# Kernel tuning notes

Hardware: AMD Instinct MI355X
Metric: run time of the kernel (lower is better)

Reference implementation:

```python
import jax, jax.numpy as jnp
import numpy as np

# Static module configuration (from init_kwargs / input_specs)
N, S, D, d, B = 256, 2, 64, 2, 64
NOUT = int(np.ceil((N - 1) / S) + 1)  # 129
NIN = N - NOUT                         # 127
EPS = 1e-60
STDDEV = 0.5


def setup_inputs() -> dict:
    key = jax.random.key(0)
    k1, k2, k3 = jax.random.split(key, 3)
    return {
        "inp": jax.random.normal(k1, (N, B, d), jnp.float32),
        "mps_input": jax.random.normal(k2, (NIN, D, D, d), jnp.float32) * STDDEV,
        "mps_output": jax.random.normal(k3, (NOUT, D, D, d, d), jnp.float32) * STDDEV,
        "training": 0,
    }


def _divide_no_nan(x, y):
    y_safe = jnp.where(y == 0, jnp.ones_like(y), y)
    return jnp.where(y == 0, jnp.zeros_like(x), x / y_safe)


def _log_norm(mps_input, mps_output):
    # Sequential transfer-matrix scan over all N sites (no samples fixed).
    Al = jnp.zeros((D, D), jnp.float32).at[0, 0].set(1.0)
    scals = []
    i_in = 0
    for i in range(N):
        amax = jnp.max(jnp.abs(Al))
        Al = Al / amax
        scals.append(amax)
        if i % S == 0 or i == N - 1:
            M = mps_output[NOUT - 1] if i == N - 1 else mps_output[i // S]  # [D,D,d,d]
            T = jnp.einsum('du,dkij->kuij', Al, M)
            Al = jnp.einsum('kuij,ulij->kl', T, M)
        else:
            M = mps_input[i_in]  # [D,D,d]
            T = jnp.einsum('du,dki->kui', Al, M)
            Al = jnp.einsum('kui,uli->kl', T, M)
            i_in += 1
    scals.append(Al[0, 0])
    return jnp.sum(jnp.log(jnp.stack(scals)))


def _forward(inp, mps_input, mps_output):
    # --- build batched site MPS (inference path: training=False, no dropout) ---
    A = jnp.einsum('bi,lrij->blrj', inp[0], mps_output[0, :1])  # [B,1,D,d]
    mps = [A]
    i_in = 0
    Al = None
    out_S = []
    for i in range(1, N - 1):
        if i % S == 0:
            x = jnp.einsum('bi,lrij->blrj', inp[i], mps_output[i // S])  # [B,D,D,d]
            A = jnp.einsum('blr,brdi->bldi', Al, x)
            Al = None
            mps.append(A)
        else:
            A = jnp.einsum('bi,lri->blr', inp[i], mps_input[i_in])  # [B,D,D]
            Al = A if Al is None else jnp.einsum('blr,brd->bld', Al, A)
            amax = jnp.max(jnp.abs(Al), axis=(1, 2), keepdims=True)
            Al = _divide_no_nan(Al, amax)
            out_S.append(amax.reshape(-1))
            i_in += 1
    x = jnp.einsum('bi,lrij->blrj', inp[N - 1], mps_output[-1][:, :1])  # [B,D,1,d]
    A = jnp.einsum('blr,brdi->bldi', Al, x) if Al is not None else x
    mps.append(A)
    out_S = 2.0 * jnp.sum(jnp.log(jnp.stack(out_S, axis=-1) + EPS), axis=1)  # [B]

    # --- contract <psi|psi> chain with per-step rescaling ---
    scals = []
    A0 = mps[0][:, 0]  # [B,D,d]
    Al = jnp.einsum('bui,bdi->bud', A0, A0)
    amax = jnp.max(jnp.abs(Al), axis=(1, 2), keepdims=True)
    Al = _divide_no_nan(Al, amax)
    scals.append(amax.reshape(-1))
    for A in mps[1:]:
        T = jnp.einsum('bdu,bdli->blui', Al, A)
        Al = jnp.einsum('blui,buri->blr', T, A)
        amax = jnp.max(jnp.abs(Al), axis=(1, 2), keepdims=True)
        Al = _divide_no_nan(Al, amax)
        scals.append(amax.reshape(-1))
    log_contr = jnp.sum(jnp.log(jnp.stack(scals, axis=-1) + EPS), axis=1)  # [B]
    logp = log_contr + jnp.log(jnp.abs(Al[:, 0, 0]) + EPS) + out_S
    return logp - _log_norm(mps_input, mps_output)


def reference(inp, mps_input, mps_output, training):
    # training==0 -> dropout disabled (faithful to call(..., training=False))
    return _forward(inp, mps_input, mps_output)
```

## Files before the change

kernel.cpp:

```cpp
#include <hip/hip_runtime.h>
#include <math.h>


typedef __attribute__((ext_vector_type(8))) short short8;
typedef __attribute__((ext_vector_type(4))) float f32x4;

#define MFMA16(a, b, c) __builtin_amdgcn_mfma_f32_16x16x32_bf16(a, b, c, 0, 0, 0)

#define ST 72
#define PL 4608
#define BS 72
#define L_AL(q) ((q) * PL)
#define L_MF(p) (2 * PL + (p) * 18432)
#define L_T     (2 * PL + 2 * 18432)
#define SU_U16  65024
#define BPL(i) ((i) * PL)

#define MINB 0ull
#define MOTB 1040384ull
#define MFIB 3153920ull
#define MFOB 4194304ull
#define WS_U16_TOT 6307840ull
#define EXPFW WS_U16_TOT
#define EXPBW (WS_U16_TOT + 4096ull)
#define EXPAF (WS_U16_TOT + 8192ull)
#define EXPW  (EXPAF + 262144ull)
#define WS_U16_ALL (EXPW + 262144ull)

#define BARRIER() do { asm volatile("s_waitcnt lgkmcnt(0)" ::: "memory"); \
                       __builtin_amdgcn_s_barrier(); } while (0)

__device__ __forceinline__ unsigned pk2(float lo, float hi) {
    unsigned r;
    asm("v_cvt_pk_bf16_f32 %0, %1, %2" : "=v"(r) : "v"(lo), "v"(hi));
    return r;
}
__device__ __forceinline__ ushort f2b(float f) {
    union { float f; unsigned u; } x; x.f = f;
    return (ushort)((x.u + 0x7FFFu + ((x.u >> 16) & 1u)) >> 16);
}
__device__ __forceinline__ float b2f(ushort h) {
    union { unsigned u; float f; } x; x.u = ((unsigned)h) << 16; return x.f;
}
__device__ __forceinline__ short8 ldfrag(const ushort* p) {
    return *reinterpret_cast<const short8*>(p);
}
__device__ __forceinline__ void st64(ushort* p, unsigned lo, unsigned hi) {
    unsigned long long v = ((unsigned long long)hi << 32) | (unsigned long long)lo;
    *reinterpret_cast<unsigned long long*>(p) = v;
}
__device__ __forceinline__ float wave_max(float v) {
#pragma unroll
    for (int off = 32; off > 0; off >>= 1) v = fmaxf(v, __shfl_xor(v, off, 64));
    return v;
}
__device__ __forceinline__ float blk_max(float v, float* scr, int tid) {
    v = wave_max(v);
    BARRIER();
    if ((tid & 63) == 0) scr[tid >> 6] = v;
    BARRIER();
    return fmaxf(fmaxf(scr[0], scr[1]), fmaxf(scr[2], scr[3]));
}
__device__ __forceinline__ short8 pk8(const float* v) {
    union { short8 s; unsigned u[4]; } r;
    r.u[0] = pk2(v[0], v[1]); r.u[1] = pk2(v[2], v[3]);
    r.u[2] = pk2(v[4], v[5]); r.u[3] = pk2(v[6], v[7]);
    return r.s;
}

__global__ __launch_bounds__(256) void preconv(const float* __restrict__ mi,
                                               const float* __restrict__ mo,
                                               ushort* __restrict__ wsb) {
    __shared__ float lf[16384];
    const int tid = threadIdx.x, blk = blockIdx.x;
    if (blk < 127) {
        const float* src = mi + (size_t)blk * 8192;
#pragma unroll
        for (int n = 0; n < 8; n++)
            *reinterpret_cast<f32x4*>(lf + 4 * (tid + 256 * n)) =
                *reinterpret_cast<const f32x4*>(src + 4 * (tid + 256 * n));
        __syncthreads();
        ushort* d1 = wsb + MINB + (size_t)blk * 8192;
        ushort* d2 = wsb + MFIB + (size_t)blk * 8192;
        const bool adj = (blk >= 64);
#pragma unroll
        for (int n = 0; n < 4; n++) {
            int c = tid + 256 * n;
            float va[8], vb[8];
            int rp = c >> 3, d0 = (c & 7) * 8;
#pragma unroll
            for (int r = 0; r < 8; r++) {
                va[r] = lf[8 * c + r];
                if (!adj) {
                    int msrc = (rp & 63) * 2 + (rp >> 6);
                    vb[r] = lf[(d0 + r) * 128 + msrc];
                } else {
                    vb[r] = lf[(rp & 63) * 128 + (d0 + r) * 2 + (rp >> 6)];
                }
            }
            *reinterpret_cast<short8*>(d1 + 8 * c) = pk8(va);
            *reinterpret_cast<short8*>(d2 + 8 * c) = pk8(vb);
        }
    } else {
        int s = blk - 127;
        const float* src = mo + (size_t)s * 16384;
#pragma unroll
        for (int n = 0; n < 16; n++)
            *reinterpret_cast<f32x4*>(lf + 4 * (tid + 256 * n)) =
                *reinterpret_cast<const f32x4*>(src + 4 * (tid + 256 * n));
        __syncthreads();
        ushort* d1 = wsb + MOTB + (size_t)s * 16384;
        ushort* d2 = wsb + MFOB + (size_t)s * 16384;
        const bool adj = (s >= 64);
#pragma unroll
        for (int n = 0; n < 8; n++) {
            int c = tid + 256 * n;
            float va[8], vb[8];
            int j = c >> 10, r = (c >> 4) & 63, dg = c & 15;
            int rp = c >> 3, d0 = (c & 7) * 8;
#pragma unroll
            for (int q = 0; q < 4; q++)
#pragma unroll
                for (int i = 0; i < 2; i++)
                    va[q * 2 + i] = lf[(dg * 4 + q) * 256 + r * 4 + i * 2 + j];
#pragma unroll
            for (int rr = 0; rr < 8; rr++) {
                if (!adj) {
                    int msrc = (rp & 63) * 4 + (rp >> 6);
                    vb[rr] = lf[(d0 + rr) * 256 + msrc];
                } else {
                    vb[rr] = lf[(rp & 63) * 256 + (d0 + rr) * 4 + (rp >> 6)];
                }
            }
            *reinterpret_cast<short8*>(d1 + 8 * c) = pk8(va);
            *reinterpret_cast<short8*>(d2 + 8 * c) = pk8(vb);
        }
    }
}

__device__ __forceinline__ void ldbf1(short8 (&bf1)[2][4], const ushort* __restrict__ mfg,
                                      int nq, int tid) {
    const int w = tid >> 6, g = (tid >> 4) & 3, l15 = tid & 15;
#pragma unroll
    for (int ks = 0; ks < 2; ks++)
#pragma unroll
        for (int tc = 0; tc < 4; tc++)
            if (tc < nq)
                bf1[ks][tc] = ldfrag(mfg + (size_t)(64 * tc + 16 * w + l15) * 64 + 32 * ks + 8 * g);
}
template <int QW, bool BFS>
__device__ __forceinline__ void ln_mm1(ushort* su, const short8 (&bf1)[2][4],
                                       int q, int p, float sc, int tid) {
    constexpr int TSx = QW * BS + 8;
    const int w = tid >> 6, g = (tid >> 4) & 3, l15 = tid & 15;
    const f32x4 fz = {0.f, 0.f, 0.f, 0.f};
    f32x4 acc[4][QW];
#pragma unroll
    for (int tr = 0; tr < 4; tr++)
#pragma unroll
        for (int tc = 0; tc < QW; tc++) acc[tr][tc] = fz;
#pragma unroll
    for (int ks = 0; ks < 2; ks++) {
        short8 bf[QW];
#pragma unroll
        for (int tc = 0; tc < QW; tc++) {
            if constexpr (BFS) bf[tc] = bf1[ks][tc];
            else bf[tc] = ldfrag(su + L_MF(p) + (64 * tc + 16 * w + l15) * ST + 32 * ks + 8 * g);
        }
#pragma unroll
        for (int tr = 0; tr < 4; tr++) {
            short8 af = ldfrag(su + L_AL(q) + (16 * tr + l15) * ST + 32 * ks + 8 * g);
#pragma unroll
            for (int tc = 0; tc < QW; tc++) acc[tr][tc] = MFMA16(af, bf[tc], acc[tr][tc]);
        }
    }
#pragma unroll
    for (int tr = 0; tr < 4; tr++)
#pragma unroll
        for (int tc = 0; tc < QW; tc++)
            st64(&su[L_T + (16 * w + l15) * TSx + tc * BS + 16 * tr + 4 * g],
                 pk2(acc[tr][tc][0] * sc, acc[tr][tc][1] * sc),
                 pk2(acc[tr][tc][2] * sc, acc[tr][tc][3] * sc));
}
template <int QW>
__device__ __forceinline__ void ln_mm2_reg(ushort* su, const short8 (&bf1)[2][4],
                                           int p, int tid, float* redw) {
    constexpr int TSx = QW * BS + 8;
    const int w = tid >> 6, g = (tid >> 4) & 3, l15 = tid & 15;
    const f32x4 fz = {0.f, 0.f, 0.f, 0.f};
    f32x4 acc[4];
#pragma unroll
    for (int tr = 0; tr < 4; tr++) acc[tr] = fz;
#pragma unroll
    for (int ks2 = 0; ks2 < 2 * QW; ks2++) {
        const short8 bf = bf1[ks2 & 1][ks2 >> 1];
#pragma unroll
        for (int tr = 0; tr < 4; tr++) {
            short8 af = ldfrag(su + L_T + (16 * tr + l15) * TSx + (ks2 >> 1) * BS +
                               (ks2 & 1) * 32 + 8 * g);
            acc[tr] = MFMA16(af, bf, acc[tr]);
        }
    }
    float lm = 0.f;
#pragma unroll
    for (int tr = 0; tr < 4; tr++)
#pragma unroll
        for (int r2 = 0; r2 < 4; r2++) lm = fmaxf(lm, fabsf(acc[tr][r2]));
    lm = wave_max(lm);
    if ((tid & 63) == 0) redw[w] = lm;
#pragma unroll
    for (int tr = 0; tr < 4; tr++)
        st64(&su[L_AL(p ^ 1) + (16 * w + l15) * ST + 16 * tr + 4 * g],
             pk2(acc[tr][0], acc[tr][1]), pk2(acc[tr][2], acc[tr][3]));
}
template <int QW>
__device__ __forceinline__ void ln_mm2_lds(ushort* su, int q, int p, int tid, float* red) {
    constexpr int TSx = QW * BS + 8;
    const int w = tid >> 6, g = (tid >> 4) & 3, l15 = tid & 15;
    const f32x4 fz = {0.f, 0.f, 0.f, 0.f};
    f32x4 acc[4];
#pragma unroll
    for (int tc = 0; tc < 4; tc++) acc[tc] = fz;
#pragma unroll
    for (int ks2 = 0; ks2 < 2 * QW; ks2++) {
        short8 af = ldfrag(su + L_T + (16 * w + l15) * TSx + (ks2 >> 1) * BS + (ks2 & 1) * 32 + 8 * g);
#pragma unroll
        for (int tc = 0; tc < 4; tc++) {
            short8 bf = ldfrag(su + L_MF(p) + (((ks2 >> 1) << 6) + 16 * tc + l15) * ST +
                               (ks2 & 1) * 32 + 8 * g);
            acc[tc] = MFMA16(af, bf, acc[tc]);
        }
    }
    float lm = 0.f;
#pragma unroll
    for (int tc = 0; tc < 4; tc++)
#pragma unroll
        for (int r2 = 0; r2 < 4; r2++) lm = fmaxf(lm, fabsf(acc[tc][r2]));
    lm = wave_max(lm);
    if ((tid & 63) == 0) red[w] = lm;
#pragma unroll
    for (int tc = 0; tc < 4; tc++)
        st64(&su[L_AL(q ^ 1) + (16 * tc + l15) * ST + 16 * w + 4 * g],
             pk2(acc[tc][0], acc[tc][1]), pk2(acc[tc][2], acc[tc][3]));
}
template <int QWN>
__device__ __forceinline__ void ln_stage_raw(ushort* su, int pn, const float* __restrict__ Mg, int tid) {
    const int a63 = tid & 63, hi = tid >> 6;
#pragma unroll
    for (int n = 0; n < 4 * QWN; n++) {
        int mb = hi + 4 * n;
        f32x4 v = *reinterpret_cast<const f32x4*>(Mg + 4 * ((size_t)a63 * (16 * QWN) + mb));
#pragma unroll
        for (int c = 0; c < 4; c++) {
            int m = 4 * mb + c;
            int rp = (m & (QWN - 1)) * 64 + (m / QWN);
            su[L_MF(pn) + rp * ST + a63] = f2b(v[c]);
        }
    }
}

__device__ __forceinline__ void bt_mm1(ushort* su, int tid) {
    const int w = tid >> 6, g = (tid >> 4) & 3, l15 = tid & 15;
    const f32x4 fz = {0.f, 0.f, 0.f, 0.f};
    f32x4 acc[2][4];
#pragma unroll
    for (int j = 0; j < 2; j++)
#pragma unroll
        for (int tr = 0; tr < 4; tr++) acc[j][tr] = fz;
#pragma unroll
    for (int ks = 0; ks < 2; ks++) {
        short8 q0 = ldfrag(su + BPL(1) + (16 * w + l15) * ST + 32 * ks + 8 * g);
        short8 q1 = ldfrag(su + BPL(2) + (16 * w + l15) * ST + 32 * ks + 8 * g);
#pragma unroll
        for (int tr = 0; tr < 4; tr++) {
            short8 pA = ldfrag(su + BPL(0) + (16 * tr + l15) * ST + 32 * ks + 8 * g);
            acc[0][tr] = MFMA16(pA, q0, acc[0][tr]);
            acc[1][tr] = MFMA16(pA, q1, acc[1][tr]);
        }
    }
#pragma unroll
    for (int j = 0; j < 2; j++)
#pragma unroll
        for (int tr = 0; tr < 4; tr++)
            st64(&su[BPL(3 + j) + (16 * w + l15) * ST + 16 * tr + 4 * g],
                 pk2(acc[j][tr][0], acc[j][tr][1]), pk2(acc[j][tr][2], acc[j][tr][3]));
}
__device__ __forceinline__ void bw_mm1(ushort* su, int tid) {
    const int w = tid >> 6, g = (tid >> 4) & 3, l15 = tid & 15;
    const f32x4 fz = {0.f, 0.f, 0.f, 0.f};
    f32x4 acc[2][4];
#pragma unroll
    for (int j = 0; j < 2; j++)
#pragma unroll
        for (int tr = 0; tr < 4; tr++) acc[j][tr] = fz;
#pragma unroll
    for (int ks = 0; ks < 2; ks++) {
        short8 bAin = ldfrag(su + BPL(0) + (16 * w + l15) * ST + 32 * ks + 8 * g);
#pragma unroll
        for (int tr = 0; tr < 4; tr++) {
            short8 x0 = ldfrag(su + BPL(1) + (16 * tr + l15) * ST + 32 * ks + 8 * g);
            short8 x1 = ldfrag(su + BPL(2) + (16 * tr + l15) * ST + 32 * ks + 8 * g);
            acc[0][tr] = MFMA16(x0, bAin, acc[0][tr]);
            acc[1][tr] = MFMA16(x1, bAin, acc[1][tr]);
        }
    }
#pragma unroll
    for (int j = 0; j < 2; j++)
#pragma unroll
        for (int tr = 0; tr < 4; tr++)
            st64(&su[BPL(3 + j) + (16 * w + l15) * ST + 16 * tr + 4 * g],
                 pk2(acc[j][tr][0], acc[j][tr][1]), pk2(acc[j][tr][2], acc[j][tr][3]));
}
__device__ __forceinline__ void bt_mm2(ushort* su, float sc, int tid) {
    const int w = tid >> 6, g = (tid >> 4) & 3, l15 = tid & 15;
    const f32x4 fz = {0.f, 0.f, 0.f, 0.f};
    f32x4 acc[2][4];
#pragma unroll
    for (int j = 0; j < 2; j++)
#pragma unroll
        for (int tr = 0; tr < 4; tr++) acc[j][tr] = fz;
#pragma unroll
    for (int ks = 0; ks < 2; ks++) {
        short8 q0 = ldfrag(su + BPL(3) + (16 * w + l15) * ST + 32 * ks + 8 * g);
        short8 q1 = ldfrag(su + BPL(4) + (16 * w + l15) * ST + 32 * ks + 8 * g);
#pragma unroll
        for (int tr = 0; tr < 4; tr++) {
            short8 pA = ldfrag(su + BPL(7) + (16 * tr + l15) * ST + 32 * ks + 8 * g);
            acc[0][tr] = MFMA16(pA, q0, acc[0][tr]);
            acc[1][tr] = MFMA16(pA, q1, acc[1][tr]);
        }
    }
#pragma unroll
    for (int j = 0; j < 2; j++)
#pragma unroll
        for (int tr = 0; tr < 4; tr++)
            st64(&su[BPL(5 + j) + (16 * w + l15) * ST + 16 * tr + 4 * g],
                 pk2(acc[j][tr][0] * sc, acc[j][tr][1] * sc),
                 pk2(acc[j][tr][2] * sc, acc[j][tr][3] * sc));
}
__device__ __forceinline__ void bt_mm3(ushort* su, int tid, float* redw) {
    const int w = tid >> 6, g = (tid >> 4) & 3, l15 = tid & 15;
    const f32x4 fz = {0.f, 0.f, 0.f, 0.f};
    f32x4 acc[4];
#pragma unroll
    for (int tc = 0; tc < 4; tc++) acc[tc] = fz;
#pragma unroll
    for (int j = 0; j < 2; j++)
#pragma unroll
        for (int ks = 0; ks < 2; ks++) {
            short8 pT = ldfrag(su + BPL(5 + j) + (16 * w + l15) * ST + 32 * ks + 8 * g);
#pragma unroll
            for (int tc = 0; tc < 4; tc++) {
                short8 qf = ldfrag(su + BPL(3 + j) + (16 * tc + l15) * ST + 32 * ks + 8 * g);
                acc[tc] = MFMA16(pT, qf, acc[tc]);
            }
        }
    float lm = 0.f;
#pragma unroll
    for (int tc = 0; tc < 4; tc++)
#pragma unroll
        for (int r2 = 0; r2 < 4; r2++) lm = fmaxf(lm, fabsf(acc[tc][r2]));
    lm = wave_max(lm);
    if ((tid & 63) == 0) redw[w] = lm;
#pragma unroll
    for (int tc = 0; tc < 4; tc++)
        st64(&su[BPL(7) + (16 * tc + l15) * ST + 16 * w + 4 * g],
             pk2(acc[tc][0], acc[tc][1]), pk2(acc[tc][2], acc[tc][3]));
}

template <bool BFS>
__global__ __launch_bounds__(256, 1) void proj_chain(
    const float* __restrict__ inp, const float* __restrict__ mps_in,
    const float* __restrict__ mps_out, float* __restrict__ wsf,
    ushort* __restrict__ wsb) {
    __shared__ __align__(16) ushort su[SU_U16];
    __shared__ float fsc[176];
    float* red = fsc;
    float* bms = fsc + 16;
    float* A0s = fsc + 32;
    const int tid = threadIdx.x;

    if (blockIdx.x >= 128) {
        if constexpr (BFS) {
            const bool fw = (blockIdx.x == 128);
#pragma unroll
            for (int n = 0; n < 9; n++)
                reinterpret_cast<unsigned*>(su)[tid + 256 * n] = 0u;
            if (tid == 0) su[0] = (ushort)0x3F80;
            auto wq = [&](int s) -> int {
                if (fw) return (s & 1) ? 2 : 4;
                int site = 255 - s;
                return (((site & 1) == 0) || site == 255) ? 4 : 2;
            };
            auto wp = [&](int s) -> const ushort* {
                if (fw) return (s & 1) ? wsb + MFIB + (size_t)(s >> 1) * 8192
                                       : wsb + MFOB + (size_t)(s >> 1) * 16384;
                int site = 255 - s;
                if (site == 255) return wsb + MFOB + 128ull * 16384;
                if ((site & 1) == 0) return wsb + MFOB + (size_t)(site >> 1) * 16384;
                return wsb + MFIB + (size_t)(site >> 1) * 8192;
            };
            short8 bfA[2][4], bfB[2][4];
            ldbf1(bfA, wp(0), wq(0), tid);
            BARRIER();
            float accl = 0.f;
            auto lnstep = [&](int s_, short8 (&CUR)[2][4], short8 (&NXT)[2][4]) {
                int p_ = s_ & 1;
                float sc_ = 1.f;
                if (s_ > 0) {
                    float* rb_ = red + p_ * 8;
                    float m4_ = fmaxf(fmaxf(rb_[0], rb_[1]), fmaxf(rb_[2], rb_[3]));
                    sc_ = 1.f / m4_;
                    if (tid == 0) accl += logf(m4_);
                }
                int q_ = wq(s_);
                if (q_ == 4) ln_mm1<4, true>(su, CUR, p_, p_, sc_, tid);
                else         ln_mm1<2, true>(su, CUR, p_, p_, sc_, tid);
                if (s_ + 1 < 128) ldbf1(NXT, wp(s_ + 1), wq(s_ + 1), tid);
                BARRIER();
                if (q_ == 4) ln_mm2_reg<4>(su, CUR, p_, tid, red + ((s_ + 1) & 1) * 8);
                else         ln_mm2_reg<2>(su, CUR, p_, tid, red + ((s_ + 1) & 1) * 8);
                BARRIER();
            };
            for (int t = 0; t < 64; ++t) {
                lnstep(2 * t, bfA, bfB);
                lnstep(2 * t + 1, bfB, bfA);
            }
            size_t base = fw ? EXPFW : EXPBW;
            int row = tid >> 2, c0 = (tid & 3) * 16;
            *reinterpret_cast<short8*>(wsb + base + row * 64 + c0) =
                ldfrag(su + (size_t)row * ST + c0);
            *reinterpret_cast<short8*>(wsb + base + row * 64 + c0 + 8) =
                ldfrag(su + (size_t)row * ST + c0 + 8);
            if (tid == 0) wsf[fw ? 128 : 129] = accl;
            return;
        } else {
            if (blockIdx.x == 129) return;
#pragma unroll
            for (int n = 0; n < 9; n++)
                reinterpret_cast<unsigned*>(su)[tid + 256 * n] = 0u;
            if (tid == 0) su[0] = (ushort)0x3F80;
            short8 bfd[2][4];
            ln_stage_raw<4>(su, 0, mps_out, tid);
            BARRIER();
            float accl = 0.f;
            for (int i = 0; i < 256; i++) {
                int p = i & 1;
                int qw = (((i & 1) == 0) || i == 255) ? 4 : 2;
                float sc = 1.f;
                if (i > 0) {
                    float* rb = red + (i & 1) * 8;
                    float m4 = fmaxf(fmaxf(rb[0], rb[1]), fmaxf(rb[2], rb[3]));
                    sc = 1.f / m4;
                    if (tid == 0) accl += logf(m4);
                }
                if (qw == 4) ln_mm1<4, false>(su, bfd, p, p, sc, tid);
                else         ln_mm1<2, false>(su, bfd, p, p, sc, tid);
                int j = i + 1;
                if (j < 256) {
                    int qn = (((j & 1) == 0) || j == 255) ? 4 : 2;
                    if (qn == 4)
                        ln_stage_raw<4>(su, p ^ 1,
                                        mps_out + (size_t)16384 * ((j == 255) ? 128 : (j >> 1)), tid);
                    else
                        ln_stage_raw<2>(su, p ^ 1, mps_in + (size_t)8192 * (j >> 1), tid);
                }
                if (qw == 4) ln_mm2_lds<4>(su, p, p, tid, red + ((i + 1) & 1) * 8);
                else         ln_mm2_lds<2>(su, p, p, tid, red + ((i + 1) & 1) * 8);
                BARRIER();
            }
            if (tid == 0) { accl += logf(b2f(su[L_AL(0)])); wsf[128] = accl; }
            return;
        }
    }

    if (!BFS && blockIdx.x >= 64) return;
    const bool FWD = (blockIdx.x < 64);
    const int b = blockIdx.x & 63;
    float accl = 0.f;
    short8 pfA[4], pfX[8];

    auto loadpf = [&](int k2) {
        const ushort* mb = wsb + MINB + (size_t)(k2 - 1) * 8192;
        const ushort* xb = wsb + MOTB + (size_t)k2 * 16384;
#pragma unroll
        for (int n = 0; n < 4; n++)
            pfA[n] = *reinterpret_cast<const short8*>(mb + (size_t)(tid + 256 * n) * 8);
#pragma unroll
        for (int n = 0; n < 8; n++)
            pfX[n] = *reinterpret_cast<const short8*>(xb + (size_t)((n >> 2) * 1024 + tid + 256 * (n & 3)) * 8);
    };
    auto stage_bf = [&](int k2) {
        float jv0 = inp[((2 * k2 - 1) * 64 + b) * 2], jv1 = inp[((2 * k2 - 1) * 64 + b) * 2 + 1];
        float ov0 = inp[((2 * k2) * 64 + b) * 2],     ov1 = inp[((2 * k2) * 64 + b) * 2 + 1];
#pragma unroll
        for (int n = 0; n < 4; n++) {
            int c = tid + 256 * n, l = c >> 4, dd0 = (c & 15) * 4;
            short8 r8 = pfA[n];
            float v0 = jv0 * b2f((ushort)r8[0]) + jv1 * b2f((ushort)r8[1]);
            float v1 = jv0 * b2f((ushort)r8[2]) + jv1 * b2f((ushort)r8[3]);
            float v2 = jv0 * b2f((ushort)r8[4]) + jv1 * b2f((ushort)r8[5]);
            float v3 = jv0 * b2f((ushort)r8[6]) + jv1 * b2f((ushort)r8[7]);
            st64(&su[BPL(0) + l * ST + dd0], pk2(v0, v1), pk2(v2, v3));
        }
#pragma unroll
        for (int n = 0; n < 8; n++) {
            int j = n >> 2, c = tid + 256 * (n & 3), r = c >> 4, dd0 = (c & 15) * 4;
            short8 r8 = pfX[n];
            float v0 = ov0 * b2f((ushort)r8[0]) + ov1 * b2f((ushort)r8[1]);
            float v1 = ov0 * b2f((ushort)r8[2]) + ov1 * b2f((ushort)r8[3]);
            float v2 = ov0 * b2f((ushort)r8[4]) + ov1 * b2f((ushort)r8[5]);
            float v3 = ov0 * b2f((ushort)r8[6]) + ov1 * b2f((ushort)r8[7]);
            st64(&su[BPL(1 + j) + r * ST + dd0], pk2(v0, v1), pk2(v2, v3));
        }
    };
    auto stage_f32 = [&](int k2) {
        const int a63 = tid & 63, hi2 = tid >> 6;
        const float* Min = mps_in + (size_t)(k2 - 1) * 8192;
        const float* Mo  = mps_out + (size_t)k2 * 16384;
        float jv0 = inp[((2 * k2 - 1) * 64 + b) * 2], jv1 = inp[((2 * k2 - 1) * 64 + b) * 2 + 1];
        float ov0 = inp[((2 * k2) * 64 + b) * 2],     ov1 = inp[((2 * k2) * 64 + b) * 2 + 1];
#pragma unroll
        for (int n = 0; n < 8; n++) {
            int f = tid + 256 * n, l = f >> 5, dd = (2 * f) & 63;
            f32x4 v = *reinterpret_cast<const f32x4*>(Min + 4 * f);
            *reinterpret_cast<unsigned*>(&su[BPL(0) + l * ST + dd]) =
                pk2(jv0 * v[0] + jv1 * v[1], jv0 * v[2] + jv1 * v[3]);
        }
#pragma unroll
        for (int n = 0; n < 16; n++) {
            int r = hi2 + 4 * n;
            f32x4 v = *reinterpret_cast<const f32x4*>(Mo + 4 * ((size_t)a63 * 64 + r));
            su[BPL(1) + r * ST + a63] = f2b(ov0 * v[0] + ov1 * v[2]);
            su[BPL(2) + r * ST + a63] = f2b(ov0 * v[1] + ov1 * v[3]);
        }
    };
    auto init_state = [&](const float* Msrc, float v0, float v1) {
        if (tid < 128) {
            int r = tid >> 1, jj = tid & 1;
            A0s[tid] = v0 * Msrc[r * 256 * 0 + r * 0 + 0] ;
        }
    };

    const int nt = FWD ? 64 : 63;
    auto sidx = [&](int t) { return FWD ? (1 + t) : (127 - t); };

    if constexpr (BFS) loadpf(sidx(0));
    {
        const float* Ms;
        float v0, v1;
        int rstride;
        if (FWD) { Ms = mps_out; v0 = inp[b * 2]; v1 = inp[b * 2 + 1]; rstride = 4; }
        else { Ms = mps_out + (size_t)128 * 16384; v0 = inp[(255 * 64 + b) * 2];
               v1 = inp[(255 * 64 + b) * 2 + 1]; rstride = 256; }
        if (tid < 128) {
            int r = tid >> 1, jj = tid & 1;
            A0s[tid] = v0 * Ms[r * rstride + jj] + v1 * Ms[r * rstride + 2 + jj];
        }
        BARRIER();
        float vals[16];
        float lm = 0.f;
#pragma unroll
        for (int n = 0; n < 16; n++) {
            int e = tid + 256 * n;
            int u = e >> 6, d2 = e & 63;
            float v = A0s[2 * u] * A0s[2 * d2] + A0s[2 * u + 1] * A0s[2 * d2 + 1];
            vals[n] = v;
            lm = fmaxf(lm, fabsf(v));
        }
        float amax = blk_max(lm, bms, tid);
        if (tid == 0) accl += logf(amax);
        float sc0 = (amax > 0.f) ? 1.f / amax : 0.f;
#pragma unroll
        for (int n = 0; n < 16; n++) {
            int e = tid + 256 * n;
            su[BPL(7) + (e >> 6) * ST + (e & 63)] = f2b(vals[n] * sc0);
        }
    }
    if (tid < 4) red[tid] = 1.0f;
    const int kmax = FWD ? (BFS ? 64 : 127) : 0;
    const int NT = BFS ? nt : 127;
    if constexpr (BFS) {
        stage_bf(sidx(0));
        if (NT > 1) loadpf(sidx(1));
    } else {
        stage_f32(1);
    }
    BARRIER();

    for (int t = 0; t < NT; t++) {
        int rb = t & 1;
        if (FWD) bt_mm1(su, tid);
        else     bw_mm1(su, tid);
        {
            float* r4 = red + rb * 4;
            float m4 = fmaxf(fmaxf(r4[0], r4[1]), fmaxf(r4[2], r4[3]));
            float sc = 1.f / m4;
            if (tid == 0) accl += logf(m4);
            bt_mm2(su, sc, tid);
        }
        BARRIER();
        if (t + 1 < NT) {
            if constexpr (BFS) stage_bf(sidx(t + 1));
            else               stage_f32(t + 2);
        }
        bt_mm3(su, tid, red + (rb ^ 1) * 4);
        if constexpr (BFS) { if (t + 2 < NT) loadpf(sidx(t + 2)); }
        BARRIER();
    }

    if constexpr (BFS) {
        size_t base = (FWD ? EXPAF : EXPW) + (size_t)b * 4096;
        int row = tid >> 2, c0 = (tid & 3) * 16;
        *reinterpret_cast<short8*>(wsb + base + row * 64 + c0) =
            ldfrag(su + BPL(7) + (size_t)row * ST + c0);
        *reinterpret_cast<short8*>(wsb + base + row * 64 + c0 + 8) =
            ldfrag(su + BPL(7) + (size_t)row * ST + c0 + 8);
        if (tid == 0) wsf[FWD ? b : 64 + b] = accl;
    } else {
        const float* Mo128 = mps_out + (size_t)128 * 16384;
        float fv0 = inp[(255 * 64 + b) * 2], fv1 = inp[(255 * 64 + b) * 2 + 1];
        if (tid < 128) {
            int d2 = tid >> 1, jj = tid & 1;
            A0s[tid] = fv0 * Mo128[d2 * 256 + jj] + fv1 * Mo128[d2 * 256 + 2 + jj];
        }
        BARRIER();
        float part = 0.f;
#pragma unroll
        for (int n = 0; n < 16; n++) {
            int e = tid + 256 * n;
            int d2 = e >> 6, u = e & 63;
            part += b2f(su[BPL(7) + d2 * ST + u]) *
                    (A0s[2 * d2] * A0s[2 * u] + A0s[2 * d2 + 1] * A0s[2 * u + 1]);
        }
#pragma unroll
        for (int off = 32; off > 0; off >>= 1)
            part += __shfl_xor(part, off, 64);
        BARRIER();
        if ((tid & 63) == 0) bms[tid >> 6] = part;
        BARRIER();
        if (tid == 0) {
            float v = bms[0] + bms[1] + bms[2] + bms[3];
            wsf[b] = accl + logf(fabsf(v));
        }
    }
}

__global__ void proj_combine(const float* __restrict__ wsf, const ushort* __restrict__ wsb,
                             float* __restrict__ out, int n, int mode) {
    __shared__ float sred[8];
    const int b = blockIdx.x, tid = threadIdx.x;
    if (b >= n) return;
    if (!mode) {
        if (tid == 0) out[b] = wsf[b] - wsf[128];
        return;
    }
    float d1 = 0.f, d2 = 0.f;
#pragma unroll
    for (int q = 0; q < 16; q++) {
        int e = tid + 256 * q;
        d1 += b2f(wsb[EXPAF + (size_t)b * 4096 + e]) * b2f(wsb[EXPW + (size_t)b * 4096 + e]);
        d2 += b2f(wsb[EXPFW + e]) * b2f(wsb[EXPBW + e]);
    }
#pragma unroll
    for (int off = 32; off > 0; off >>= 1) {
        d1 += __shfl_xor(d1, off, 64);
        d2 += __shfl_xor(d2, off, 64);
    }
    if ((tid & 63) == 0) { sred[tid >> 6] = d1; sred[4 + (tid >> 6)] = d2; }
    __syncthreads();
    if (tid == 0) {
        float D1 = sred[0] + sred[1] + sred[2] + sred[3];
        float D2 = sred[4] + sred[5] + sred[6] + sred[7];
        out[b] = wsf[b] + wsf[64 + b] + logf(fabsf(D1)) -
                 (wsf[128] + wsf[129] + logf(fabsf(D2)));
    }
}

extern "C" void kernel_launch(void* const* d_in, const int* in_sizes, int n_in,
                              void* d_out, int out_size, void* d_ws, size_t ws_size,
                              hipStream_t stream) {
    const float* inp = (const float*)d_in[0];
    const float* mi  = (const float*)d_in[1];
    const float* mo  = (const float*)d_in[2];
    float* wsf = (float*)d_ws;
    ushort* wsb = (ushort*)((char*)d_ws + 1024);
    size_t need = 1024 + WS_U16_ALL * 2;
    int mode = (ws_size >= need) ? 1 : 0;
    if (mode) {
        preconv<<<dim3(256), dim3(256), 0, stream>>>(mi, mo, wsb);
        proj_chain<true><<<dim3(130), dim3(256), 0, stream>>>(inp, mi, mo, wsf, wsb);
    } else {
        proj_chain<false><<<dim3(130), dim3(256), 0, stream>>>(inp, mi, mo, wsf, wsb);
    }
    proj_combine<<<dim3(64), dim3(256), 0, stream>>>(wsf, wsb, (float*)d_out, out_size, mode);
}
```

Before: 316.1 us.

## Stage log-norm weights through LDS with register prefetch, split MFMA accumulators

The log-norm scan blocks stop holding the site weights as per-wave register fragments loaded straight from global memory. They now stage each site's weights into a double-buffered LDS slot, prefetching the site two steps ahead into registers. The second matmul reads weights from LDS, which leaves one barrier per step instead of two. The mm2 and bt_mm3 kernels also split their MFMA accumulation into two independent chains to shorten dependency stalls, at the cost of extra registers and an add. Unused helper code is removed.

```diff
diff --git a/kernel.cpp b/kernel.cpp
--- a/kernel.cpp
+++ b/kernel.cpp
@@ -138,17 +138,7 @@
     }
 }
 
-__device__ __forceinline__ void ldbf1(short8 (&bf1)[2][4], const ushort* __restrict__ mfg,
-                                      int nq, int tid) {
-    const int w = tid >> 6, g = (tid >> 4) & 3, l15 = tid & 15;
-#pragma unroll
-    for (int ks = 0; ks < 2; ks++)
-#pragma unroll
-        for (int tc = 0; tc < 4; tc++)
-            if (tc < nq)
-                bf1[ks][tc] = ldfrag(mfg + (size_t)(64 * tc + 16 * w + l15) * 64 + 32 * ks + 8 * g);
-}
-template <int QW, bool BFS>
+template <int QW, bool REGW>
 __device__ __forceinline__ void ln_mm1(ushort* su, const short8 (&bf1)[2][4],
                                        int q, int p, float sc, int tid) {
     constexpr int TSx = QW * BS + 8;
@@ -164,7 +154,7 @@
         short8 bf[QW];
 #pragma unroll
         for (int tc = 0; tc < QW; tc++) {
-            if constexpr (BFS) bf[tc] = bf1[ks][tc];
+            if constexpr (REGW) bf[tc] = bf1[ks][tc];
             else bf[tc] = ldfrag(su + L_MF(p) + (64 * tc + 16 * w + l15) * ST + 32 * ks + 8 * g);
         }
 #pragma unroll
@@ -181,46 +171,15 @@
             st64(&su[L_T + (16 * w + l15) * TSx + tc * BS + 16 * tr + 4 * g],
                  pk2(acc[tr][tc][0] * sc, acc[tr][tc][1] * sc),
                  pk2(acc[tr][tc][2] * sc, acc[tr][tc][3] * sc));
-}
-template <int QW>
-__device__ __forceinline__ void ln_mm2_reg(ushort* su, const short8 (&bf1)[2][4],
-                                           int p, int tid, float* redw) {
-    constexpr int TSx = QW * BS + 8;
-    const int w = tid >> 6, g = (tid >> 4) & 3, l15 = tid & 15;
-    const f32x4 fz = {0.f, 0.f, 0.f, 0.f};
-    f32x4 acc[4];
-#pragma unroll
-    for (int tr = 0; tr < 4; tr++) acc[tr] = fz;
-#pragma unroll
-    for (int ks2 = 0; ks2 < 2 * QW; ks2++) {
-        const short8 bf = bf1[ks2 & 1][ks2 >> 1];
-#pragma unroll
-        for (int tr = 0; tr < 4; tr++) {
-            short8 af = ldfrag(su + L_T + (16 * tr + l15) * TSx + (ks2 >> 1) * BS +
-                               (ks2 & 1) * 32 + 8 * g);
-            acc[tr] = MFMA16(af, bf, acc[tr]);
-        }
-    }
-    float lm = 0.f;
-#pragma unroll
-    for (int tr = 0; tr < 4; tr++)
-#pragma unroll
-        for (int r2 = 0; r2 < 4; r2++) lm = fmaxf(lm, fabsf(acc[tr][r2]));
-    lm = wave_max(lm);
-    if ((tid & 63) == 0) redw[w] = lm;
-#pragma unroll
-    for (int tr = 0; tr < 4; tr++)
-        st64(&su[L_AL(p ^ 1) + (16 * w + l15) * ST + 16 * tr + 4 * g],
-             pk2(acc[tr][0], acc[tr][1]), pk2(acc[tr][2], acc[tr][3]));
 }
 template <int QW>
 __device__ __forceinline__ void ln_mm2_lds(ushort* su, int q, int p, int tid, float* red) {
     constexpr int TSx = QW * BS + 8;
     const int w = tid >> 6, g = (tid >> 4) & 3, l15 = tid & 15;
     const f32x4 fz = {0.f, 0.f, 0.f, 0.f};
-    f32x4 acc[4];
-#pragma unroll
-    for (int tc = 0; tc < 4; tc++) acc[tc] = fz;
+    f32x4 accA[4], accB[4];
+#pragma unroll
+    for (int tc = 0; tc < 4; tc++) { accA[tc] = fz; accB[tc] = fz; }
 #pragma unroll
     for (int ks2 = 0; ks2 < 2 * QW; ks2++) {
         short8 af = ldfrag(su + L_T + (16 * w + l15) * TSx + (ks2 >> 1) * BS + (ks2 & 1) * 32 + 8 * g);
@@ -228,9 +187,13 @@
         for (int tc = 0; tc < 4; tc++) {
             short8 bf = ldfrag(su + L_MF(p) + (((ks2 >> 1) << 6) + 16 * tc + l15) * ST +
                                (ks2 & 1) * 32 + 8 * g);
-            acc[tc] = MFMA16(af, bf, acc[tc]);
-        }
-    }
+            if (ks2 & 1) accB[tc] = MFMA16(af, bf, accB[tc]);
+            else         accA[tc] = MFMA16(af, bf, accA[tc]);
+        }
+    }
+    f32x4 acc[4];
+#pragma unroll
+    for (int tc = 0; tc < 4; tc++) acc[tc] = accA[tc] + accB[tc];
     float lm = 0.f;
 #pragma unroll
     for (int tc = 0; tc < 4; tc++)
@@ -341,9 +304,11 @@
 __device__ __forceinline__ void bt_mm3(ushort* su, int tid, float* redw) {
     const int w = tid >> 6, g = (tid >> 4) & 3, l15 = tid & 15;
     const f32x4 fz = {0.f, 0.f, 0.f, 0.f};
-    f32x4 acc[4];
-#pragma unroll
-    for (int tc = 0; tc < 4; tc++) acc[tc] = fz;
+    f32x4 accJ[2][4];
+#pragma unroll
+    for (int j = 0; j < 2; j++)
+#pragma unroll
+        for (int tc = 0; tc < 4; tc++) accJ[j][tc] = fz;
 #pragma unroll
     for (int j = 0; j < 2; j++)
 #pragma unroll
@@ -352,9 +317,12 @@
 #pragma unroll
             for (int tc = 0; tc < 4; tc++) {
                 short8 qf = ldfrag(su + BPL(3 + j) + (16 * tc + l15) * ST + 32 * ks + 8 * g);
-                acc[tc] = MFMA16(pT, qf, acc[tc]);
+                accJ[j][tc] = MFMA16(pT, qf, accJ[j][tc]);
             }
         }
+    f32x4 acc[4];
+#pragma unroll
+    for (int tc = 0; tc < 4; tc++) acc[tc] = accJ[0][tc] + accJ[1][tc];
     float lm = 0.f;
 #pragma unroll
     for (int tc = 0; tc < 4; tc++)
@@ -381,6 +349,7 @@
     const int tid = threadIdx.x;
 
     if (blockIdx.x >= 128) {
+        short8 bfd[2][4];
         if constexpr (BFS) {
             const bool fw = (blockIdx.x == 128);
 #pragma unroll
@@ -400,31 +369,58 @@
                 if ((site & 1) == 0) return wsb + MFOB + (size_t)(site >> 1) * 16384;
                 return wsb + MFIB + (size_t)(site >> 1) * 8192;
             };
-            short8 bfA[2][4], bfB[2][4];
-            ldbf1(bfA, wp(0), wq(0), tid);
+            short8 pf[8];
+            {
+                const ushort* s0 = wp(0);
+                int q0 = wq(0);
+#pragma unroll
+                for (int n = 0; n < 8; n++)
+                    if (n < 2 * q0) {
+                        int c = tid + 256 * n;
+                        *reinterpret_cast<short8*>(su + L_MF(0) + (c >> 3) * ST + (c & 7) * 8) =
+                            *reinterpret_cast<const short8*>(s0 + (size_t)c * 8);
+                    }
+                const ushort* s1 = wp(1);
+                int q1 = wq(1);
+#pragma unroll
+                for (int n = 0; n < 8; n++)
+                    if (n < 2 * q1)
+                        pf[n] = *reinterpret_cast<const short8*>(s1 + (size_t)(tid + 256 * n) * 8);
+            }
             BARRIER();
             float accl = 0.f;
-            auto lnstep = [&](int s_, short8 (&CUR)[2][4], short8 (&NXT)[2][4]) {
-                int p_ = s_ & 1;
-                float sc_ = 1.f;
-                if (s_ > 0) {
-                    float* rb_ = red + p_ * 8;
-                    float m4_ = fmaxf(fmaxf(rb_[0], rb_[1]), fmaxf(rb_[2], rb_[3]));
-                    sc_ = 1.f / m4_;
-                    if (tid == 0) accl += logf(m4_);
+            for (int s = 0; s < 128; s++) {
+                int p = s & 1;
+                int qw = wq(s);
+                float sc = 1.f;
+                if (s > 0) {
+                    float* rb = red + p * 8;
+                    float m4 = fmaxf(fmaxf(rb[0], rb[1]), fmaxf(rb[2], rb[3]));
+                    sc = 1.f / m4;
+                    if (tid == 0) accl += logf(m4);
                 }
-                int q_ = wq(s_);
-                if (q_ == 4) ln_mm1<4, true>(su, CUR, p_, p_, sc_, tid);
-                else         ln_mm1<2, true>(su, CUR, p_, p_, sc_, tid);
-                if (s_ + 1 < 128) ldbf1(NXT, wp(s_ + 1), wq(s_ + 1), tid);
+                if (qw == 4) ln_mm1<4, false>(su, bfd, p, p, sc, tid);
+                else         ln_mm1<2, false>(su, bfd, p, p, sc, tid);
+                if (s + 1 < 128) {
+                    int qn = wq(s + 1);
+#pragma unroll
+                    for (int n = 0; n < 8; n++)
+                        if (n < 2 * qn) {
+                            int c = tid + 256 * n;
+                            *reinterpret_cast<short8*>(su + L_MF(p ^ 1) + (c >> 3) * ST + (c & 7) * 8) = pf[n];
+                        }
+                }
+                if (s + 2 < 128) {
+                    int q2 = wq(s + 2);
+                    const ushort* s2 = wp(s + 2);
+#pragma unroll
+                    for (int n = 0; n < 8; n++)
+                        if (n < 2 * q2)
+                            pf[n] = *reinterpret_cast<const short8*>(s2 + (size_t)(tid + 256 * n) * 8);
+                }
+                if (qw == 4) ln_mm2_lds<4>(su, p, p, tid, red + ((s + 1) & 1) * 8);
+                else         ln_mm2_lds<2>(su, p, p, tid, red + ((s + 1) & 1) * 8);
                 BARRIER();
-                if (q_ == 4) ln_mm2_reg<4>(su, CUR, p_, tid, red + ((s_ + 1) & 1) * 8);
-                else         ln_mm2_reg<2>(su, CUR, p_, tid, red + ((s_ + 1) & 1) * 8);
-                BARRIER();
-            };
-            for (int t = 0; t < 64; ++t) {
-                lnstep(2 * t, bfA, bfB);
-                lnstep(2 * t + 1, bfB, bfA);
             }
             size_t base = fw ? EXPFW : EXPBW;
             int row = tid >> 2, c0 = (tid & 3) * 16;
@@ -440,7 +436,6 @@
             for (int n = 0; n < 9; n++)
                 reinterpret_cast<unsigned*>(su)[tid + 256 * n] = 0u;
             if (tid == 0) su[0] = (ushort)0x3F80;
-            short8 bfd[2][4];
             ln_stage_raw<4>(su, 0, mps_out, tid);
             BARRIER();
             float accl = 0.f;
@@ -535,12 +530,6 @@
             su[BPL(2) + r * ST + a63] = f2b(ov0 * v[1] + ov1 * v[3]);
         }
     };
-    auto init_state = [&](const float* Msrc, float v0, float v1) {
-        if (tid < 128) {
-            int r = tid >> 1, jj = tid & 1;
-            A0s[tid] = v0 * Msrc[r * 256 * 0 + r * 0 + 0] ;
-        }
-    };
 
     const int nt = FWD ? 64 : 63;
     auto sidx = [&](int t) { return FWD ? (1 + t) : (127 - t); };
@@ -578,7 +567,6 @@
         }
     }
     if (tid < 4) red[tid] = 1.0f;
-    const int kmax = FWD ? (BFS ? 64 : 127) : 0;
     const int NT = BFS ? nt : 127;
     if constexpr (BFS) {
         stage_bf(sidx(0));
```

Measured after the change: 270.4 us, median of 2. -14.4%, faster.
